# Kernel optimization log

Measured on AMD Instinct MI355X. Metric: run time of the kernel, lower is better.

Reference implementation:

```python
import jax, jax.numpy as jnp
import numpy as np

S, B, H = 4096, 1, 2048       # [seq, batch, hidden] layout (NeoX convention)
NP, HN = 16, H // 16          # heads, head dim
ROT = int(HN * 0.25)          # rotary_ndims = 32 (rotary_pct=0.25)
ROPE_BASE = 10000.0


def setup_inputs() -> dict:
    key = jax.random.key(0)
    k0, k1, k2 = jax.random.split(key, 3)
    hidden_states = jax.random.normal(k0, (S, B, H), jnp.float32) * 0.02
    # causal left-to-right mask: True = masked out (filled with -10000)
    attention_mask = jnp.triu(jnp.ones((1, 1, S, S), bool), k=1)
    w_qkv = jax.random.normal(k1, (3 * H, H), jnp.float32) * (1.0 / np.sqrt(H))
    w_dense = jax.random.normal(k2, (H, H), jnp.float32) * (1.0 / np.sqrt(H))
    b_dense = jnp.zeros((H,), jnp.float32)
    return {"hidden_states": hidden_states, "attention_mask": attention_mask,
            "w_qkv": w_qkv, "w_dense": w_dense, "b_dense": b_dense}


def _apply_rope(x, pos):
    # x: [s, b, np, ROT]; NeoX rotate_half convention
    inv_freq = 1.0 / (ROPE_BASE ** (jnp.arange(0, ROT, 2, dtype=jnp.float32) / ROT))
    freqs = pos[:, None] * inv_freq[None, :]              # [s, ROT/2]
    emb = jnp.concatenate([freqs, freqs], axis=-1)        # [s, ROT]
    cos = jnp.cos(emb)[:, None, None, :]
    sin = jnp.sin(emb)[:, None, None, :]
    x1, x2 = jnp.split(x, 2, axis=-1)
    rot = jnp.concatenate([-x2, x1], axis=-1)
    return x * cos + rot * sin


def reference(hidden_states, attention_mask, w_qkv, w_dense, b_dense):
    s, b, h = hidden_states.shape
    # fused QKV projection (no bias), reshape to [s, b, np, 3*hn], split
    qkv = (hidden_states @ w_qkv.T).reshape(s, b, NP, 3 * HN)
    q, k, v = jnp.split(qkv, 3, axis=-1)                  # each [s, b, np, hn]
    # partial rotary embedding on first ROT dims
    pos = jnp.arange(s, dtype=jnp.float32)
    q = jnp.concatenate([_apply_rope(q[..., :ROT], pos), q[..., ROT:]], axis=-1)
    k = jnp.concatenate([_apply_rope(k[..., :ROT], pos), k[..., ROT:]], axis=-1)
    # raw attention scores [b, np, s_q, s_k], scale 1/sqrt(hn)
    scores = jnp.einsum('sbhd,tbhd->bhst', q, k) / np.float32(np.sqrt(HN))
    # ltor mask: fill masked positions with -10000, softmax in fp32
    scores = jnp.where(attention_mask, jnp.float32(-10000.0), scores)
    probs = jax.nn.softmax(scores.astype(jnp.float32), axis=-1).astype(hidden_states.dtype)
    # context [s, b, np, hn] -> [s, b, h]
    ctx = jnp.einsum('bhst,tbhd->sbhd', probs, v).reshape(s, b, h)
    return ctx @ w_dense.T + b_dense
```

## Files before the change

### kernel.cpp

```cpp
#include <hip/hip_runtime.h>

#define S_LEN 4096
#define HID   2048
#define NHEAD 16
#define HDIM  128
#define QSCALE_L2E 0.12751664352f

typedef float  f32x4  __attribute__((ext_vector_type(4)));
typedef float  f32x16 __attribute__((ext_vector_type(16)));
typedef __bf16 bf16x8 __attribute__((ext_vector_type(8)));
typedef unsigned u32x4 __attribute__((ext_vector_type(4)));
typedef unsigned u32x2 __attribute__((ext_vector_type(2)));

#define MFMA16(a, b, c) __builtin_amdgcn_mfma_f32_16x16x32_bf16((a), (b), (c), 0, 0, 0)
#define MFMA32(a, b, c) __builtin_amdgcn_mfma_f32_32x32x16_bf16((a), (b), (c), 0, 0, 0)

__device__ __forceinline__ void gld16(const void* g, void* l) {
  __builtin_amdgcn_global_load_lds(
      (const __attribute__((address_space(1))) void*)(unsigned long long)(g),
      (__attribute__((address_space(3))) void*)(unsigned long long)(l),
      16, 0, 0);
}

__device__ __forceinline__ unsigned short f2bf(float f) {
  union { float f; unsigned u; } v; v.f = f;
  unsigned r = v.u + 0x7FFFu + ((v.u >> 16) & 1u);
  return (unsigned short)(r >> 16);
}
__device__ __forceinline__ float bf2f(unsigned short h) {
  union { unsigned u; float f; } v; v.u = ((unsigned)h) << 16;
  return v.f;
}
__device__ __forceinline__ unsigned cvtpk_bf16(float a, float b) {
  unsigned r;
  asm("v_cvt_pk_bf16_f32 %0, %1, %2" : "=v"(r) : "v"(a), "v"(b));
  return r;
}
__device__ __forceinline__ u32x2 pls(unsigned a, unsigned b) {
  return __builtin_amdgcn_permlane32_swap(a, b, false, false);
}
__device__ __forceinline__ float asf(unsigned u) { return __builtin_bit_cast(float, u); }
__device__ __forceinline__ unsigned asu(float f) { return __builtin_bit_cast(unsigned, f); }

__global__ __launch_bounds__(256) void cvt_kernel(const float* __restrict__ src,
                                                  unsigned short* __restrict__ dst, int n) {
  int i = (blockIdx.x * 256 + threadIdx.x) * 4;
  if (i >= n) return;
  const float4 v = *(const float4*)(src + i);
  ushort4 o;
  o.x = f2bf(v.x); o.y = f2bf(v.y); o.z = f2bf(v.z); o.w = f2bf(v.w);
  *(ushort4*)(dst + i) = o;
}

__global__ __launch_bounds__(256, 3) void gemm_qkv_kernel(
    const unsigned short* __restrict__ A, const unsigned short* __restrict__ B,
    unsigned short* __restrict__ Qb, unsigned short* __restrict__ Kb,
    unsigned short* __restrict__ Vt) {
  __shared__ __align__(16) unsigned short As[2][128 * 32];
  __shared__ __align__(16) unsigned short Bs[2][128 * 32];
  const int K = HID;
  const int bid = ((int)blockIdx.x % 8) * 192 + (int)blockIdx.x / 8;
  const int bm = bid / 48, bn = bid % 48;
  const int row0 = bm * 128, col0 = bn * 128;
  const int tid = threadIdx.x;
  const int wid = tid >> 6, lane = tid & 63;
  const int g = lane >> 4, r16 = lane & 15;
  const int wr = wid >> 1, wc = wid & 1;

  f32x4 acc[4][4] = {};

  int srow[2], scol[2];
#pragma unroll
  for (int c = 0; c < 2; ++c) {
    int byteoff = (wid * 2 + c) * 1024 + lane * 16;
    srow[c] = byteoff >> 6;
    scol[c] = (byteoff & 63) >> 1;
  }

  auto stage = [&](int buf, int t) {
    const int k0 = t * 32;
#pragma unroll
    for (int c = 0; c < 2; ++c) {
      gld16(A + (row0 + srow[c]) * K + k0 + scol[c], &As[buf][(wid * 2 + c) * 512]);
      gld16(B + (col0 + srow[c]) * K + k0 + scol[c], &Bs[buf][(wid * 2 + c) * 512]);
    }
  };

  const int nt = K / 32;
  stage(0, 0);
  __syncthreads();
  for (int t = 0; t < nt; ++t) {
    const int cur = t & 1;
    if (t + 1 < nt) stage(cur ^ 1, t + 1);
    const char* as = (const char*)As[cur];
    const char* bs = (const char*)Bs[cur];
    bf16x8 af[4], bfv[4];
#pragma unroll
    for (int m = 0; m < 4; ++m)
      af[m] = *(const bf16x8*)(as + (wr * 64 + m * 16 + r16) * 64 + g * 16);
#pragma unroll
    for (int n = 0; n < 4; ++n)
      bfv[n] = *(const bf16x8*)(bs + (wc * 64 + n * 16 + r16) * 64 + g * 16);
#pragma unroll
    for (int m = 0; m < 4; ++m)
#pragma unroll
      for (int n = 0; n < 4; ++n)
        acc[m][n] = MFMA16(af[m], bfv[n], acc[m][n]);
    __syncthreads();
  }

  const int type = bn % 3, p = bn / 3;
#pragma unroll
  for (int m = 0; m < 4; ++m) {
    const int s0 = row0 + wr * 64 + m * 16 + g * 4;
#pragma unroll
    for (int n = 0; n < 4; ++n) {
      const int d = wc * 64 + n * 16 + r16;
      if (type == 0) {
#pragma unroll
        for (int r = 0; r < 4; ++r)
          Qb[(p * S_LEN + s0 + r) * HDIM + d] = f2bf(acc[m][n][r] * QSCALE_L2E);
      } else if (type == 1) {
#pragma unroll
        for (int r = 0; r < 4; ++r)
          Kb[(p * S_LEN + s0 + r) * HDIM + d] = f2bf(acc[m][n][r]);
      } else {
        ushort4 o;
        o.x = f2bf(acc[m][n][0]); o.y = f2bf(acc[m][n][1]);
        o.z = f2bf(acc[m][n][2]); o.w = f2bf(acc[m][n][3]);
        *(ushort4*)(Vt + (p * HDIM + d) * S_LEN + s0) = o;
      }
    }
  }
}

__global__ __launch_bounds__(256) void rope_kernel(unsigned short* __restrict__ Qb,
                                                   unsigned short* __restrict__ Kb) {
  const int idx = blockIdx.x * 256 + threadIdx.x;
  const int p = idx >> 16, rem = idx & 65535, s = rem >> 4, d = rem & 15;
  const float invf = exp2f(-(float)d * (13.287712379549449f / 16.0f));
  const float ang = (float)s * invf;
  const float c = cosf(ang), sn = sinf(ang);
  const int base = (p * S_LEN + s) * HDIM;
  {
    float x = bf2f(Qb[base + d]), y = bf2f(Qb[base + d + 16]);
    Qb[base + d]      = f2bf(x * c - y * sn);
    Qb[base + d + 16] = f2bf(y * c + x * sn);
  }
  {
    float x = bf2f(Kb[base + d]), y = bf2f(Kb[base + d + 16]);
    Kb[base + d]      = f2bf(x * c - y * sn);
    Kb[base + d + 16] = f2bf(y * c + x * sn);
  }
}

__global__ __launch_bounds__(256, 2) void attn_kernel(
    const unsigned short* __restrict__ Qb, const unsigned short* __restrict__ Kb,
    const unsigned short* __restrict__ Vt, unsigned short* __restrict__ Ctx) {
  __shared__ __align__(16) unsigned char sm[81920];
  const int b = (int)blockIdx.x;
  const int p = b & 15;
  const int qt = (b < 256) ? (b >> 4) : 47 - (b >> 4);
  const int tid = threadIdx.x, wid = tid >> 6, lane = tid & 63;
  const int l31 = lane & 31, hi = lane >> 5;
  const int xr = (l31 & 7) << 4;

  const int q0w = qt * 128 + wid * 32;
  const int qg = q0w + l31;
  const int nt = 2 * (qt + 1);
  const int np = nt >> 1;

  auto stage = [&](int t, int ko, int vo) {
    const unsigned short* kb = Kb + (p * S_LEN + t * 64) * HDIM;
    const unsigned short* vb = Vt + p * HDIM * S_LEN + t * 64;
#pragma unroll
    for (int c = 0; c < 4; ++c) {
      const int chunk = c * 256 + tid;
      const int byteoff = chunk * 16;
      const int j = byteoff >> 8, cbK = (byteoff >> 4) & 15;
      gld16(kb + j * HDIM + (cbK ^ (j & 7)) * 8, sm + ko + chunk * 16);
      const int dd = byteoff >> 7, cbV = (byteoff >> 4) & 7;
      gld16(vb + dd * S_LEN + (cbV ^ (dd & 7)) * 8, sm + vo + chunk * 16);
    }
  };

  bf16x8 qf[8];
  f32x16 acc[4] = {};
  float m_s = -1e30f, l_s = 0.f;

  auto qk = [&](f32x16& s0, f32x16& s1, const unsigned char* kl) {
    __builtin_amdgcn_s_setprio(1);
#pragma unroll
    for (int dd = 0; dd < 8; ++dd) {
      bf16x8 k0 = *(const bf16x8*)(kl + l31 * 256 + (((dd * 2 + hi) << 4) ^ xr));
      bf16x8 k1 = *(const bf16x8*)(kl + (32 + l31) * 256 + (((dd * 2 + hi) << 4) ^ xr));
      s0 = MFMA32(k0, qf[dd], s0);
      s1 = MFMA32(k1, qf[dd], s1);
    }
    __builtin_amdgcn_s_setprio(0);
  };

  auto smpv = [&](f32x16& s0, f32x16& s1, int t, int vo) {
    const unsigned char* vl = sm + vo;
    if (t * 64 + 63 > q0w) {
#pragma unroll
      for (int r = 0; r < 16; ++r) {
        const int kv0 = t * 64 + ((r & 3) + 8 * (r >> 2)) + 4 * hi;
        if (kv0 > qg) s0[r] = -1e30f;
        if (kv0 + 32 > qg) s1[r] = -1e30f;
      }
    }
    float mx[16];
#pragma unroll
    for (int r = 0; r < 16; ++r) mx[r] = fmaxf(s0[r], s1[r]);
#pragma unroll
    for (int r = 0; r < 8; ++r) mx[r] = fmaxf(mx[r], mx[r + 8]);
#pragma unroll
    for (int r = 0; r < 4; ++r) mx[r] = fmaxf(mx[r], mx[r + 4]);
    mx[0] = fmaxf(fmaxf(mx[0], mx[2]), fmaxf(mx[1], mx[3]));
    float pm;
    {
      u32x2 e = pls(asu(mx[0]), asu(mx[0]));
      pm = fmaxf(asf(e.x), asf(e.y));
    }
    if (__any(pm > m_s + 11.5f)) {
      const float mn = fmaxf(m_s, pm);
      const float scl = exp2f(m_s - mn);
#pragma unroll
      for (int d32 = 0; d32 < 4; ++d32)
#pragma unroll
        for (int r = 0; r < 16; ++r) acc[d32][r] *= scl;
      l_s *= scl;
      m_s = mn;
    }
#pragma unroll
    for (int r = 0; r < 16; ++r) {
      s0[r] = exp2f(s0[r] - m_s);
      s1[r] = exp2f(s1[r] - m_s);
    }
    bf16x8 pf[4];
#define PACKB(B, SV, base)                                                        \
    {                                                                             \
      unsigned X0 = cvtpk_bf16(SV[base + 0], SV[base + 1]);                       \
      unsigned X1 = cvtpk_bf16(SV[base + 2], SV[base + 3]);                       \
      unsigned Y0 = cvtpk_bf16(SV[base + 4], SV[base + 5]);                       \
      unsigned Y1 = cvtpk_bf16(SV[base + 6], SV[base + 7]);                       \
      u32x2 e0 = pls(X0, Y0);                                                     \
      u32x2 e1 = pls(X1, Y1);                                                     \
      u32x4 pw;                                                                   \
      pw.x = e0.x; pw.y = e1.x; pw.z = e0.y; pw.w = e1.y;                         \
      pf[B] = __builtin_bit_cast(bf16x8, pw);                                     \
    }
    PACKB(0, s0, 0)
    PACKB(1, s0, 8)
    PACKB(2, s1, 0)
    PACKB(3, s1, 8)
#undef PACKB
    __builtin_amdgcn_s_setprio(1);
#pragma unroll
    for (int d32 = 0; d32 < 4; ++d32) {
#pragma unroll
      for (int bb = 0; bb < 4; ++bb) {
        bf16x8 vf = *(const bf16x8*)(vl + (d32 * 32 + l31) * 128 + (((bb * 2 + hi) << 4) ^ xr));
        acc[d32] = MFMA32(vf, pf[bb], acc[d32]);
      }
    }
    __builtin_amdgcn_s_setprio(0);
    float s_[8];
#pragma unroll
    for (int r = 0; r < 8; ++r) s_[r] = (s0[r] + s0[r + 8]) + (s1[r] + s1[r + 8]);
#pragma unroll
    for (int r = 0; r < 4; ++r) s_[r] += s_[r + 4];
    const float rs = (s_[0] + s_[1]) + (s_[2] + s_[3]);
    u32x2 e = pls(asu(rs), asu(rs));
    l_s += asf(e.x) + asf(e.y);
  };

  stage(0, 0, 32768);
  stage(1, 16384, 49152);
  {
    const unsigned short* qp_ = Qb + (p * S_LEN + qg) * HDIM + hi * 8;
#pragma unroll
    for (int dd = 0; dd < 8; ++dd) qf[dd] = *(const bf16x8*)(qp_ + dd * 16);
  }
  int vcur = 32768, vnext = 49152, vstage = 65536;
  __syncthreads();
  f32x16 sA0 = {}, sA1 = {};
  qk(sA0, sA1, sm);
  __syncthreads();

  for (int tt = 0; tt < np; ++tt) {
    const bool more = (tt + 1 < np);
    const int t = 2 * tt;
    f32x16 sB0 = {}, sB1 = {};
    qk(sB0, sB1, sm + 16384);
    if (more) stage(t + 2, 0, vstage);
    smpv(sA0, sA1, t, vcur);
    { int tmp = vcur; vcur = vnext; vnext = vstage; vstage = tmp; }
    __syncthreads();
    if (more) {
      sA0 = {}; sA1 = {};
      qk(sA0, sA1, sm);
      stage(t + 3, 16384, vstage);
    }
    smpv(sB0, sB1, t + 1, vcur);
    { int tmp = vcur; vcur = vnext; vnext = vstage; vstage = tmp; }
    __syncthreads();
  }

  const float inv = 1.0f / l_s;
  unsigned short* cbase = Ctx + qg * HID + p * HDIM;
#pragma unroll
  for (int d32 = 0; d32 < 4; ++d32)
#pragma unroll
    for (int r = 0; r < 16; ++r) {
      const int d = d32 * 32 + ((r & 3) + 8 * (r >> 2)) + 4 * hi;
      cbase[d] = f2bf(acc[d32][r] * inv);
    }
}

__global__ __launch_bounds__(256, 3) void gemm_dense_kernel(
    const unsigned short* __restrict__ A, const unsigned short* __restrict__ B,
    const float* __restrict__ bias, float* __restrict__ out) {
  __shared__ __align__(16) unsigned short As[2][128 * 32];
  __shared__ __align__(16) unsigned short Bs[2][128 * 32];
  const int K = HID;
  const int bid = ((int)blockIdx.x % 8) * 64 + (int)blockIdx.x / 8;
  const int bm = bid / 16, bn = bid % 16;
  const int row0 = bm * 128, col0 = bn * 128;
  const int tid = threadIdx.x;
  const int wid = tid >> 6, lane = tid & 63;
  const int g = lane >> 4, r16 = lane & 15;
  const int wr = wid >> 1, wc = wid & 1;

  f32x4 acc[4][4] = {};

  int srow[2], scol[2];
#pragma unroll
  for (int c = 0; c < 2; ++c) {
    int byteoff = (wid * 2 + c) * 1024 + lane * 16;
    srow[c] = byteoff >> 6;
    scol[c] = (byteoff & 63) >> 1;
  }
  auto stage = [&](int buf, int t) {
    const int k0 = t * 32;
#pragma unroll
    for (int c = 0; c < 2; ++c) {
      gld16(A + (row0 + srow[c]) * K + k0 + scol[c], &As[buf][(wid * 2 + c) * 512]);
      gld16(B + (col0 + srow[c]) * K + k0 + scol[c], &Bs[buf][(wid * 2 + c) * 512]);
    }
  };

  const int nt = K / 32;
  stage(0, 0);
  __syncthreads();
  for (int t = 0; t < nt; ++t) {
    const int cur = t & 1;
    if (t + 1 < nt) stage(cur ^ 1, t + 1);
    const char* as = (const char*)As[cur];
    const char* bs = (const char*)Bs[cur];
    bf16x8 af[4], bfv[4];
#pragma unroll
    for (int m = 0; m < 4; ++m)
      af[m] = *(const bf16x8*)(as + (wr * 64 + m * 16 + r16) * 64 + g * 16);
#pragma unroll
    for (int n = 0; n < 4; ++n)
      bfv[n] = *(const bf16x8*)(bs + (wc * 64 + n * 16 + r16) * 64 + g * 16);
#pragma unroll
    for (int m = 0; m < 4; ++m)
#pragma unroll
      for (int n = 0; n < 4; ++n)
        acc[m][n] = MFMA16(af[m], bfv[n], acc[m][n]);
    __syncthreads();
  }

#pragma unroll
  for (int m = 0; m < 4; ++m) {
    const int s0 = row0 + wr * 64 + m * 16 + g * 4;
#pragma unroll
    for (int n = 0; n < 4; ++n) {
      const int col = col0 + wc * 64 + n * 16 + r16;
      const float bv = bias[col];
#pragma unroll
      for (int r = 0; r < 4; ++r)
        out[(s0 + r) * HID + col] = acc[m][n][r] + bv;
    }
  }
}

extern "C" void kernel_launch(void* const* d_in, const int* in_sizes, int n_in,
                              void* d_out, int out_size, void* d_ws, size_t ws_size,
                              hipStream_t stream) {
  (void)in_sizes; (void)n_in; (void)out_size; (void)ws_size;
  const float* hidden = (const float*)d_in[0];
  const float* wqkv   = (const float*)d_in[2];
  const float* wdense = (const float*)d_in[3];
  const float* bdense = (const float*)d_in[4];
  float* out = (float*)d_out;

  char* ws = (char*)d_ws;
  unsigned short* hiddenB = (unsigned short*)(ws);
  unsigned short* wqkvB   = (unsigned short*)(ws + 16777216);
  unsigned short* wdenseB = (unsigned short*)(ws + 41943040);
  unsigned short* Qb      = (unsigned short*)(ws + 50331648);
  unsigned short* Kb      = (unsigned short*)(ws + 67108864);
  unsigned short* Vt      = (unsigned short*)(ws + 83886080);
  unsigned short* ctxB    = (unsigned short*)(ws + 100663296);

  cvt_kernel<<<8192, 256, 0, stream>>>(hidden, hiddenB, 8388608);
  cvt_kernel<<<12288, 256, 0, stream>>>(wqkv, wqkvB, 12582912);
  cvt_kernel<<<4096, 256, 0, stream>>>(wdense, wdenseB, 4194304);
  gemm_qkv_kernel<<<1536, 256, 0, stream>>>(hiddenB, wqkvB, Qb, Kb, Vt);
  rope_kernel<<<4096, 256, 0, stream>>>(Qb, Kb);
  attn_kernel<<<512, 256, 0, stream>>>(Qb, Kb, Vt, ctxB);
  gemm_dense_kernel<<<512, 256, 0, stream>>>(ctxB, wdenseB, bdense, out);
}
```

Before: 331.0 us.

## Merge QKV and dense GEMMs into a 256x128-tile, 512-thread kernel with swizzled LDS

Replaces the two 128x128, BK=32 GEMM kernels with one templated kernel. It uses 256x128 output tiles, 8 waves per block, BK=64 double buffering and an XOR-swizzled LDS layout to avoid bank conflicts. The K step is split into two halves so the next tile's A and B loads can be issued between MFMA phases, with s_setprio raised during MFMA. This aims for more data reuse per LDS byte and better overlap of loads with compute. The cost is 96KB of LDS per block and fewer blocks for the smaller dense GEMM, which can lower occupancy.

Measured after the change: 316.2 us. -4.5%, faster.

```diff
diff --git a/kernel.cpp b/kernel.cpp
--- a/kernel.cpp
+++ b/kernel.cpp
@@ -52,83 +52,138 @@
   *(ushort4*)(dst + i) = o;
 }
 
-__global__ __launch_bounds__(256, 3) void gemm_qkv_kernel(
+template <int EPI>
+__global__ __launch_bounds__(512, 2) void gemm256_kernel(
     const unsigned short* __restrict__ A, const unsigned short* __restrict__ B,
     unsigned short* __restrict__ Qb, unsigned short* __restrict__ Kb,
-    unsigned short* __restrict__ Vt) {
-  __shared__ __align__(16) unsigned short As[2][128 * 32];
-  __shared__ __align__(16) unsigned short Bs[2][128 * 32];
-  const int K = HID;
-  const int bid = ((int)blockIdx.x % 8) * 192 + (int)blockIdx.x / 8;
-  const int bm = bid / 48, bn = bid % 48;
-  const int row0 = bm * 128, col0 = bn * 128;
+    unsigned short* __restrict__ Vt,
+    const float* __restrict__ bias, float* __restrict__ out) {
+  __shared__ __align__(16) unsigned char sm[98304];
+  constexpr int K = HID;
+  constexpr int NT = K / 64;
+  constexpr int NB = (EPI == 0) ? 768 : 256;
+  const int b = (int)blockIdx.x;
+  const int swz = (b & 7) * (NB >> 3) + (b >> 3);
+  const int bm = swz & 15, bn = swz >> 4;
+  const int row0 = bm * 256, col0 = bn * 128;
   const int tid = threadIdx.x;
   const int wid = tid >> 6, lane = tid & 63;
   const int g = lane >> 4, r16 = lane & 15;
-  const int wr = wid >> 1, wc = wid & 1;
+  const int wm = wid >> 1, wn = wid & 1;
+
+  auto stageA = [&](int t) {
+    const int bufo = (t & 1) * 49152;
+    const int k0 = t * 64;
+#pragma unroll
+    for (int h = 0; h < 2; ++h)
+#pragma unroll
+      for (int cc = 0; cc < 2; ++cc) {
+        const int chunk = cc * 512 + tid;
+        const int r = chunk >> 3, c7 = chunk & 7;
+        gld16(A + (row0 + h * 128 + r) * K + k0 + ((c7 ^ (r & 7)) << 3),
+              sm + bufo + h * 16384 + chunk * 16);
+      }
+  };
+  auto stageB = [&](int t) {
+    const int bufo = (t & 1) * 49152;
+    const int k0 = t * 64;
+#pragma unroll
+    for (int cc = 0; cc < 2; ++cc) {
+      const int chunk = cc * 512 + tid;
+      const int r = chunk >> 3, c7 = chunk & 7;
+      gld16(B + (col0 + r) * K + k0 + ((c7 ^ (r & 7)) << 3),
+            sm + bufo + 32768 + chunk * 16);
+    }
+  };
 
   f32x4 acc[4][4] = {};
 
-  int srow[2], scol[2];
-#pragma unroll
-  for (int c = 0; c < 2; ++c) {
-    int byteoff = (wid * 2 + c) * 1024 + lane * 16;
-    srow[c] = byteoff >> 6;
-    scol[c] = (byteoff & 63) >> 1;
-  }
-
-  auto stage = [&](int buf, int t) {
-    const int k0 = t * 32;
-#pragma unroll
-    for (int c = 0; c < 2; ++c) {
-      gld16(A + (row0 + srow[c]) * K + k0 + scol[c], &As[buf][(wid * 2 + c) * 512]);
-      gld16(B + (col0 + srow[c]) * K + k0 + scol[c], &Bs[buf][(wid * 2 + c) * 512]);
-    }
-  };
-
-  const int nt = K / 32;
-  stage(0, 0);
-  __syncthreads();
-  for (int t = 0; t < nt; ++t) {
-    const int cur = t & 1;
-    if (t + 1 < nt) stage(cur ^ 1, t + 1);
-    const char* as = (const char*)As[cur];
-    const char* bs = (const char*)Bs[cur];
+  int aoff[4], boff[4];
+#pragma unroll
+  for (int m = 0; m < 4; ++m) {
+    const int r = (wm & 1) * 64 + m * 16 + r16;
+    aoff[m] = (wm >> 1) * 16384 + r * 128 + ((g * 16) ^ ((r & 7) << 4));
+  }
+#pragma unroll
+  for (int n = 0; n < 4; ++n) {
+    const int r = wn * 64 + n * 16 + r16;
+    boff[n] = 32768 + r * 128 + ((g * 16) ^ ((r & 7) << 4));
+  }
+
+  stageA(0); stageB(0);
+  asm volatile("s_waitcnt vmcnt(0)" ::: "memory");
+  __builtin_amdgcn_s_barrier();
+
+  for (int t = 0; t < NT; ++t) {
+    const int bufo = (t & 1) * 49152;
+    const bool st = (t + 1 < NT);
     bf16x8 af[4], bfv[4];
 #pragma unroll
+    for (int m = 0; m < 4; ++m) af[m] = *(const bf16x8*)(sm + bufo + aoff[m]);
+#pragma unroll
+    for (int n = 0; n < 4; ++n) bfv[n] = *(const bf16x8*)(sm + bufo + boff[n]);
+    if (st) stageA(t + 1);
+    __builtin_amdgcn_s_barrier();
+    asm volatile("s_waitcnt lgkmcnt(0)" ::: "memory");
+    __builtin_amdgcn_s_setprio(1);
+#pragma unroll
     for (int m = 0; m < 4; ++m)
-      af[m] = *(const bf16x8*)(as + (wr * 64 + m * 16 + r16) * 64 + g * 16);
-#pragma unroll
-    for (int n = 0; n < 4; ++n)
-      bfv[n] = *(const bf16x8*)(bs + (wc * 64 + n * 16 + r16) * 64 + g * 16);
+#pragma unroll
+      for (int n = 0; n < 4; ++n) acc[m][n] = MFMA16(af[m], bfv[n], acc[m][n]);
+    __builtin_amdgcn_s_setprio(0);
+    __builtin_amdgcn_s_barrier();
+#pragma unroll
+    for (int m = 0; m < 4; ++m) af[m] = *(const bf16x8*)(sm + bufo + (aoff[m] ^ 64));
+#pragma unroll
+    for (int n = 0; n < 4; ++n) bfv[n] = *(const bf16x8*)(sm + bufo + (boff[n] ^ 64));
+    if (st) stageB(t + 1);
+    __builtin_amdgcn_s_barrier();
+    asm volatile("s_waitcnt lgkmcnt(0)" ::: "memory");
+    __builtin_amdgcn_s_setprio(1);
 #pragma unroll
     for (int m = 0; m < 4; ++m)
 #pragma unroll
-      for (int n = 0; n < 4; ++n)
-        acc[m][n] = MFMA16(af[m], bfv[n], acc[m][n]);
-    __syncthreads();
-  }
-
-  const int type = bn % 3, p = bn / 3;
-#pragma unroll
-  for (int m = 0; m < 4; ++m) {
-    const int s0 = row0 + wr * 64 + m * 16 + g * 4;
-#pragma unroll
-    for (int n = 0; n < 4; ++n) {
-      const int d = wc * 64 + n * 16 + r16;
-      if (type == 0) {
+      for (int n = 0; n < 4; ++n) acc[m][n] = MFMA16(af[m], bfv[n], acc[m][n]);
+    __builtin_amdgcn_s_setprio(0);
+    if (st) asm volatile("s_waitcnt vmcnt(0)" ::: "memory");
+    __builtin_amdgcn_s_barrier();
+  }
+
+  if constexpr (EPI == 0) {
+    const int type = bn % 3, p = bn / 3;
+#pragma unroll
+    for (int m = 0; m < 4; ++m) {
+      const int s0 = row0 + wm * 64 + m * 16 + g * 4;
+#pragma unroll
+      for (int n = 0; n < 4; ++n) {
+        const int d = wn * 64 + n * 16 + r16;
+        if (type == 0) {
+#pragma unroll
+          for (int r = 0; r < 4; ++r)
+            Qb[(p * S_LEN + s0 + r) * HDIM + d] = f2bf(acc[m][n][r] * QSCALE_L2E);
+        } else if (type == 1) {
+#pragma unroll
+          for (int r = 0; r < 4; ++r)
+            Kb[(p * S_LEN + s0 + r) * HDIM + d] = f2bf(acc[m][n][r]);
+        } else {
+          ushort4 o;
+          o.x = f2bf(acc[m][n][0]); o.y = f2bf(acc[m][n][1]);
+          o.z = f2bf(acc[m][n][2]); o.w = f2bf(acc[m][n][3]);
+          *(ushort4*)(Vt + (p * HDIM + d) * S_LEN + s0) = o;
+        }
+      }
+    }
+  } else {
+#pragma unroll
+    for (int m = 0; m < 4; ++m) {
+      const int s0 = row0 + wm * 64 + m * 16 + g * 4;
+#pragma unroll
+      for (int n = 0; n < 4; ++n) {
+        const int col = col0 + wn * 64 + n * 16 + r16;
+        const float bv = bias[col];
 #pragma unroll
         for (int r = 0; r < 4; ++r)
-          Qb[(p * S_LEN + s0 + r) * HDIM + d] = f2bf(acc[m][n][r] * QSCALE_L2E);
-      } else if (type == 1) {
-#pragma unroll
-        for (int r = 0; r < 4; ++r)
-          Kb[(p * S_LEN + s0 + r) * HDIM + d] = f2bf(acc[m][n][r]);
-      } else {
-        ushort4 o;
-        o.x = f2bf(acc[m][n][0]); o.y = f2bf(acc[m][n][1]);
-        o.z = f2bf(acc[m][n][2]); o.w = f2bf(acc[m][n][3]);
-        *(ushort4*)(Vt + (p * HDIM + d) * S_LEN + s0) = o;
+          out[(s0 + r) * HID + col] = acc[m][n][r] + bv;
       }
     }
   }
@@ -319,75 +374,6 @@
     }
 }
 
-__global__ __launch_bounds__(256, 3) void gemm_dense_kernel(
-    const unsigned short* __restrict__ A, const unsigned short* __restrict__ B,
-    const float* __restrict__ bias, float* __restrict__ out) {
-  __shared__ __align__(16) unsigned short As[2][128 * 32];
-  __shared__ __align__(16) unsigned short Bs[2][128 * 32];
-  const int K = HID;
-  const int bid = ((int)blockIdx.x % 8) * 64 + (int)blockIdx.x / 8;
-  const int bm = bid / 16, bn = bid % 16;
-  const int row0 = bm * 128, col0 = bn * 128;
-  const int tid = threadIdx.x;
-  const int wid = tid >> 6, lane = tid & 63;
-  const int g = lane >> 4, r16 = lane & 15;
-  const int wr = wid >> 1, wc = wid & 1;
-
-  f32x4 acc[4][4] = {};
-
-  int srow[2], scol[2];
-#pragma unroll
-  for (int c = 0; c < 2; ++c) {
-    int byteoff = (wid * 2 + c) * 1024 + lane * 16;
-    srow[c] = byteoff >> 6;
-    scol[c] = (byteoff & 63) >> 1;
-  }
-  auto stage = [&](int buf, int t) {
-    const int k0 = t * 32;
-#pragma unroll
-    for (int c = 0; c < 2; ++c) {
-      gld16(A + (row0 + srow[c]) * K + k0 + scol[c], &As[buf][(wid * 2 + c) * 512]);
-      gld16(B + (col0 + srow[c]) * K + k0 + scol[c], &Bs[buf][(wid * 2 + c) * 512]);
-    }
-  };
-
-  const int nt = K / 32;
-  stage(0, 0);
-  __syncthreads();
-  for (int t = 0; t < nt; ++t) {
-    const int cur = t & 1;
-    if (t + 1 < nt) stage(cur ^ 1, t + 1);
-    const char* as = (const char*)As[cur];
-    const char* bs = (const char*)Bs[cur];
-    bf16x8 af[4], bfv[4];
-#pragma unroll
-    for (int m = 0; m < 4; ++m)
-      af[m] = *(const bf16x8*)(as + (wr * 64 + m * 16 + r16) * 64 + g * 16);
-#pragma unroll
-    for (int n = 0; n < 4; ++n)
-      bfv[n] = *(const bf16x8*)(bs + (wc * 64 + n * 16 + r16) * 64 + g * 16);
-#pragma unroll
-    for (int m = 0; m < 4; ++m)
-#pragma unroll
-      for (int n = 0; n < 4; ++n)
-        acc[m][n] = MFMA16(af[m], bfv[n], acc[m][n]);
-    __syncthreads();
-  }
-
-#pragma unroll
-  for (int m = 0; m < 4; ++m) {
-    const int s0 = row0 + wr * 64 + m * 16 + g * 4;
-#pragma unroll
-    for (int n = 0; n < 4; ++n) {
-      const int col = col0 + wc * 64 + n * 16 + r16;
-      const float bv = bias[col];
-#pragma unroll
-      for (int r = 0; r < 4; ++r)
-        out[(s0 + r) * HID + col] = acc[m][n][r] + bv;
-    }
-  }
-}
-
 extern "C" void kernel_launch(void* const* d_in, const int* in_sizes, int n_in,
                               void* d_out, int out_size, void* d_ws, size_t ws_size,
                               hipStream_t stream) {
@@ -410,8 +396,8 @@
   cvt_kernel<<<8192, 256, 0, stream>>>(hidden, hiddenB, 8388608);
   cvt_kernel<<<12288, 256, 0, stream>>>(wqkv, wqkvB, 12582912);
   cvt_kernel<<<4096, 256, 0, stream>>>(wdense, wdenseB, 4194304);
-  gemm_qkv_kernel<<<1536, 256, 0, stream>>>(hiddenB, wqkvB, Qb, Kb, Vt);
+  gemm256_kernel<0><<<768, 512, 0, stream>>>(hiddenB, wqkvB, Qb, Kb, Vt, nullptr, nullptr);
   rope_kernel<<<4096, 256, 0, stream>>>(Qb, Kb);
   attn_kernel<<<512, 256, 0, stream>>>(Qb, Kb, Vt, ctxB);
-  gemm_dense_kernel<<<512, 256, 0, stream>>>(ctxB, wdenseB, bdense, out);
-}
+  gemm256_kernel<1><<<256, 512, 0, stream>>>(ctxB, wdenseB, nullptr, nullptr, nullptr, bdense, out);
+}
```
